# Kernel optimization log

Measured on AMD Instinct MI355X. Metric: run time of the kernel, lower is better.

The kernel has to match this reference:

```python
import jax, jax.numpy as jnp
import numpy as np

D = 1024   # feature_dim
K = 10     # num_anchors
B = 16384  # batch
H = 8      # num_heads


def setup_inputs() -> dict:
    key = jax.random.key(0)
    ks = jax.random.split(key, 12)
    f32 = jnp.float32

    def w(k, shape, scale=0.02):
        return (jax.random.normal(k, shape, f32) * scale)

    return {
        "features": jax.random.normal(ks[0], (B, D), f32),
        "anchors": w(ks[1], (K, D), 0.1),
        # anchor_refiner: Linear(D, D//2) -> ReLU -> Linear(D//2, D) -> Tanh
        "ar_w1": w(ks[2], (D, D // 2)), "ar_b1": jnp.zeros((D // 2,), f32),
        "ar_w2": w(ks[3], (D // 2, D)), "ar_b2": jnp.zeros((D,), f32),
        # attention projections
        "q_w": w(ks[4], (D, D)), "q_b": jnp.zeros((D,), f32),
        "k_w": w(ks[5], (D, D)), "k_b": jnp.zeros((D,), f32),
        "v_w": w(ks[6], (D, D)), "v_b": jnp.zeros((D,), f32),
        "o_w": w(ks[7], (D, D)), "o_b": jnp.zeros((D,), f32),
        # feature_enhancer: LayerNorm -> Linear(D,2D) -> GELU -> Linear(2D,D)
        "ln_g": jnp.ones((D,), f32), "ln_b": jnp.zeros((D,), f32),
        "ff_w1": w(ks[8], (D, 2 * D)), "ff_b1": jnp.zeros((2 * D,), f32),
        "ff_w2": w(ks[9], (2 * D, D)), "ff_b2": jnp.zeros((D,), f32),
        "div_w": jnp.asarray(0.001, f32),
        "cen_w": jnp.asarray(0.001, f32),
    }


def _l2norm(x, eps=1e-8):
    n = jnp.linalg.norm(x, axis=-1, keepdims=True)
    return x / jnp.maximum(n, eps)


def _layernorm(x, g, b, eps=1e-5):
    mu = jnp.mean(x, axis=-1, keepdims=True)
    var = jnp.mean(jnp.square(x - mu), axis=-1, keepdims=True)
    return (x - mu) * jax.lax.rsqrt(var + eps) * g + b


def reference(features, anchors, ar_w1, ar_b1, ar_w2, ar_b2,
              q_w, q_b, k_w, k_b, v_w, v_b, o_w, o_b,
              ln_g, ln_b, ff_w1, ff_b1, ff_w2, ff_b2, div_w, cen_w):
    b = features.shape[0]
    hd = D // H
    fn = _l2norm(features)                                 # [B, D]

    # anchor refinement
    refin = jnp.tanh(jax.nn.relu(anchors @ ar_w1 + ar_b1) @ ar_w2 + ar_b2)
    an = _l2norm(anchors + 0.1 * refin)                    # [K, D]

    # multi-head cross-attention to anchors
    q = (fn @ q_w + q_b).reshape(b, H, hd)                 # [B, H, hd]
    k = (an @ k_w + k_b).reshape(K, H, hd)                 # [K, H, hd]
    v = (an @ v_w + v_b).reshape(K, H, hd)
    scores = jnp.einsum('bhd,khd->bhk', q, k) / jnp.sqrt(jnp.asarray(hd, fn.dtype))
    aw = jax.nn.softmax(scores, axis=-1)                   # [B, H, K]
    att = jnp.einsum('bhk,khd->bhd', aw, v).reshape(b, D)
    att = att @ o_w + o_b

    # feature enhancer (dropout inactive: eval mode)
    enh = fn + 0.1 * att
    h = jax.nn.gelu(_layernorm(enh, ln_g, ln_b) @ ff_w1 + ff_b1, approximate=False)
    enh = h @ ff_w2 + ff_b2
    final = fn + 0.2 * enh                                 # [B, D]

    # diversity loss: pdist over K=10 anchors (45 pairs)
    diff = an[:, None, :] - an[None, :, :]                 # [K, K, D]
    dmat = jnp.sqrt(jnp.maximum(jnp.sum(diff * diff, -1), 1e-24))
    iu = np.triu_indices(K, 1)
    div_loss = jnp.exp(-jnp.maximum(dmat[iu].mean(), 1e-6))

    # center loss: attention-weighted feature-anchor distances
    avg_att = aw.mean(axis=1)                              # [B, K]
    sq = (jnp.sum(fn * fn, 1, keepdims=True) + jnp.sum(an * an, 1)
          - 2.0 * fn @ an.T)
    fa_dist = jnp.sqrt(jnp.maximum(sq, 1e-12))             # [B, K]
    center_loss = jnp.sum(avg_att * fa_dist, axis=1).mean()

    geo = jnp.abs(div_w) * div_loss + jnp.abs(cen_w) * center_loss
    geo = jnp.clip(geo, 0.0, 0.01)
    return final, geo
```

## Files before the change

### kernel.cpp

```cpp
#include <hip/hip_runtime.h>
#include <hip/hip_bf16.h>
#include <math.h>

typedef __hip_bfloat16 bf16;

#define D_  1024
#define K_  10
#define B_  16384
#define H_  8
#define HD_ 128

struct alignas(16) BF8 { bf16 v[8]; };
struct alignas(8)  BF4 { bf16 v[4]; };

typedef __bf16 bf8v __attribute__((ext_vector_type(8)));
typedef float  f4v  __attribute__((ext_vector_type(4)));

__device__ __forceinline__ float b2f(bf16 x){ return __bfloat162float(x); }
__device__ __forceinline__ bf16  f2b(float x){ return __float2bfloat16(x); }

#define GL2LDS16(g, l) __builtin_amdgcn_global_load_lds( \
    (__attribute__((address_space(1))) void*)(g), \
    (__attribute__((address_space(3))) void*)(l), 16, 0, 0)

__global__ __launch_bounds__(256) void l2norm_k(const float* __restrict__ x,
                                                bf16* __restrict__ fnb) {
  int b = blockIdx.x, t = threadIdx.x;
  float4 v = ((const float4*)(x + (size_t)b * D_))[t];
  float p = v.x*v.x + v.y*v.y + v.z*v.z + v.w*v.w;
  #pragma unroll
  for (int o = 32; o > 0; o >>= 1) p += __shfl_down(p, o);
  __shared__ float wsum[4];
  if ((t & 63) == 0) wsum[t >> 6] = p;
  __syncthreads();
  __shared__ float inv_s;
  if (t == 0) inv_s = 1.f / fmaxf(sqrtf(wsum[0]+wsum[1]+wsum[2]+wsum[3]), 1e-8f);
  __syncthreads();
  float iv = inv_s;
  BF4 o;
  o.v[0] = f2b(v.x*iv); o.v[1] = f2b(v.y*iv);
  o.v[2] = f2b(v.z*iv); o.v[3] = f2b(v.w*iv);
  ((BF4*)(fnb + (size_t)b * D_))[t] = o;
}

__global__ __launch_bounds__(256) void wt_k(const float* __restrict__ w,
                                            bf16* __restrict__ wt, int R, int C) {
  __shared__ float tle[32][33];
  int c0 = blockIdx.x * 32, r0 = blockIdx.y * 32;
  int tx = threadIdx.x & 31, ty = threadIdx.x >> 5;
  #pragma unroll
  for (int i = 0; i < 32; i += 8)
    tle[ty + i][tx] = w[(size_t)(r0 + ty + i) * C + c0 + tx];
  __syncthreads();
  #pragma unroll
  for (int i = 0; i < 32; i += 8)
    wt[(size_t)(c0 + ty + i) * R + r0 + tx] = f2b(tle[tx][ty + i]);
}

template<int COLS, int KD, int ACT>
__global__ __launch_bounds__(256) void panelmm_k(
    const float* __restrict__ A, const float* __restrict__ W,
    const float* __restrict__ bias, const float* __restrict__ aux,
    float* __restrict__ out,
    const float* __restrict__ W2, const float* __restrict__ bias2,
    float* __restrict__ out2, int N, int npanel) {
  constexpr int GROUPS = 256 / COLS;
  constexpr int DCH = KD / GROUPS;
  __shared__ float A_s[K_][KD];
  __shared__ float part[K_][COLS][GROUPS];
  const int t = threadIdx.x;
  int blk = blockIdx.x;
  const float* Wm = W; const float* bm = bias; float* om = out;
  if (blk >= npanel) { blk -= npanel; Wm = W2; bm = bias2; om = out2; }
  const int panel = blk;
  for (int i = t; i < K_*KD; i += 256) A_s[0][i] = A[i];
  __syncthreads();
  const int cg = t % COLS, g = t / COLS;
  const int col = panel*COLS + cg;
  float s[K_];
  #pragma unroll
  for (int r = 0; r < K_; ++r) s[r] = 0.f;
  const float* wp = Wm + (size_t)(g*DCH)*N + col;
  for (int d = g*DCH; d < (g+1)*DCH; ++d) {
    float wv = *wp; wp += N;
    #pragma unroll
    for (int r = 0; r < K_; ++r) s[r] = fmaf(A_s[r][d], wv, s[r]);
  }
  #pragma unroll
  for (int r = 0; r < K_; ++r) part[r][cg][g] = s[r];
  __syncthreads();
  for (int o = t; o < K_*COLS; o += 256) {
    int r = o / COLS, c = o % COLS;
    float v = 0.f;
    #pragma unroll
    for (int gg = 0; gg < GROUPS; ++gg) v += part[r][c][gg];
    v += bm[panel*COLS + c];
    if constexpr (ACT == 1) v = fmaxf(v, 0.f);
    if constexpr (ACT == 2) v = aux[(size_t)r*N + panel*COLS + c] + 0.1f*tanhf(v);
    om[(size_t)r*N + panel*COLS + c] = v;
  }
}

template<int TRANSOUT, typename TW>
__global__ __launch_bounds__(256) void smallmm_k(
    const float* __restrict__ A, const TW* __restrict__ W,
    bf16* __restrict__ outb, float scale) {
  constexpr int COLS = 64, GROUPS = 4, DCH = 32, NW = 1024;
  __shared__ float A_s[K_][128];
  __shared__ float part[K_][COLS][GROUPS];
  const int t = threadIdx.x;
  const int h = blockIdx.x & 7, panel = blockIdx.x >> 3;
  for (int i = t; i < K_*128; i += 256) {
    int r = i >> 7, j = i & 127;
    A_s[r][j] = A[r*1024 + h*128 + j];
  }
  __syncthreads();
  const int cg = t % COLS, g = t / COLS;
  const int col = panel*COLS + cg;
  float s[K_];
  #pragma unroll
  for (int r = 0; r < K_; ++r) s[r] = 0.f;
  const TW* wp = W + (size_t)(h*128 + g*DCH)*NW + col;
  for (int d = g*DCH; d < g*DCH + DCH; ++d) {
    float wv;
    if constexpr (sizeof(TW) == 2) wv = b2f(*wp); else wv = *wp;
    wp += NW;
    #pragma unroll
    for (int r = 0; r < K_; ++r) s[r] = fmaf(A_s[r][d], wv, s[r]);
  }
  #pragma unroll
  for (int r = 0; r < K_; ++r) part[r][cg][g] = s[r];
  __syncthreads();
  for (int o = t; o < 16*COLS; o += 256) {
    int r = o / COLS, c = o % COLS;
    float v = 0.f;
    if (r < K_) {
      #pragma unroll
      for (int gg = 0; gg < GROUPS; ++gg) v += part[r][c][gg];
      v *= scale;
    }
    if constexpr (TRANSOUT) outb[(size_t)(panel*COLS + c)*128 + h*16 + r] = f2b(v);
    else                    outb[(size_t)(h*16 + r)*NW + panel*COLS + c] = f2b(v);
  }
}

__global__ void sbias_k(const float* __restrict__ qb, const float* __restrict__ Km,
                        float* __restrict__ sb) {
  int c = threadIdx.x;
  int h = c >> 4, k = c & 15;
  float s = 0.f;
  if (k < K_) {
    for (int j = 0; j < HD_; ++j)
      s = fmaf(qb[h*HD_ + j], Km[(size_t)k*D_ + h*HD_ + j], s);
  }
  sb[c] = s * 0.08838834764831845f;
}

__global__ __launch_bounds__(256) void ar3_k(const float* __restrict__ an_un,
    float* __restrict__ an, float* __restrict__ na, float* __restrict__ divloss) {
  __shared__ float a_s[K_][D_];
  __shared__ float nrm[K_];
  __shared__ float dm[45];
  const int t = threadIdx.x;
  for (int i = t; i < K_*D_; i += 256) a_s[0][i] = an_un[i];
  __syncthreads();
  const int wid = t >> 6, lane = t & 63;
  for (int r = wid; r < K_; r += 4) {
    float p = 0.f;
    for (int j = lane; j < D_; j += 64) p += a_s[r][j]*a_s[r][j];
    #pragma unroll
    for (int o = 1; o < 64; o <<= 1) p += __shfl_xor(p, o);
    if (lane == 0) nrm[r] = p;
  }
  __syncthreads();
  for (int i = t; i < K_*D_; i += 256) {
    int r = i >> 10;
    float iv = 1.f / fmaxf(sqrtf(nrm[r]), 1e-8f);
    float v = a_s[0][i] * iv;
    a_s[0][i] = v;
    an[i] = v;
  }
  if (t < K_) {
    float iv = 1.f / fmaxf(sqrtf(nrm[t]), 1e-8f);
    na[t] = nrm[t] * iv * iv;
  }
  __syncthreads();
  const int pr = t >> 2, sub = t & 3;
  if (pr < 45) {
    int i = 0, j = 0, c = pr;
    for (i = 0; i < K_; ++i) { int cnt = K_-1-i; if (c < cnt) { j = i+1+c; break; } c -= cnt; }
    float s = 0.f;
    for (int d = sub*256; d < sub*256 + 256; ++d) {
      float df = a_s[i][d] - a_s[j][d]; s += df*df;
    }
    s += __shfl_xor(s, 1); s += __shfl_xor(s, 2);
    if (sub == 0) dm[pr] = sqrtf(fmaxf(s, 1e-24f));
  }
  __syncthreads();
  if (t == 0) {
    float m = 0.f;
    for (int p = 0; p < 45; ++p) m += dm[p];
    m *= (1.f/45.f);
    *divloss = expf(-fmaxf(m, 1e-6f));
  }
}

template<int EPI, typename TO>
__global__ __launch_bounds__(256) void mgemm_k(
    const bf16* __restrict__ A, const bf16* __restrict__ Bt,
    const float* __restrict__ bias, const bf16* __restrict__ aux,
    TO* __restrict__ out, int M, int N, int Kd, float scale) {
  constexpr int BM = 128, BN = 128, BK = 32;
  __shared__ bf16 As[BM][BK];
  __shared__ bf16 Bs[BN][BK];
  const int tid = threadIdx.x;
  const int nMB = M / BM;
  const int nwg = gridDim.x;
  int wg = blockIdx.x;
  wg = (wg & 7) * (nwg >> 3) + (wg >> 3);
  const int mb = wg % nMB, nb = wg / nMB;
  const int bm = mb * BM, bn = nb * BN;

  const int srow = tid >> 2;
  const int sk   = (tid & 3) * 8;
  const bf16* ga = A  + (size_t)(bm + srow) * Kd + sk;
  const bf16* gb = Bt + (size_t)(bn + srow) * Kd + sk;
  const size_t rstep = (size_t)64 * Kd;
  bf16* la = &As[0][0] + tid * 8;
  bf16* lb = &Bs[0][0] + tid * 8;

  const int w    = tid >> 6;
  const int lane = tid & 63;
  const int wr = (w >> 1) * 64, wc = (w & 1) * 64;
  const int fr = lane & 15, fg = lane >> 4;

  f4v acc[4][4];
  const f4v zz = {0.f, 0.f, 0.f, 0.f};
  #pragma unroll
  for (int m = 0; m < 4; ++m)
    #pragma unroll
    for (int n = 0; n < 4; ++n) acc[m][n] = zz;

  for (int k0 = 0; k0 < Kd; k0 += BK) {
    GL2LDS16(ga,         la);
    GL2LDS16(ga + rstep, la + 2048);
    GL2LDS16(gb,         lb);
    GL2LDS16(gb + rstep, lb + 2048);
    __syncthreads();
    bf8v af[4], bf_[4];
    #pragma unroll
    for (int m = 0; m < 4; ++m)
      af[m] = *(const bf8v*)&As[wr + m*16 + fr][fg*8];
    #pragma unroll
    for (int n = 0; n < 4; ++n)
      bf_[n] = *(const bf8v*)&Bs[wc + n*16 + fr][fg*8];
    #pragma unroll
    for (int m = 0; m < 4; ++m)
      #pragma unroll
      for (int n = 0; n < 4; ++n)
        acc[m][n] = __builtin_amdgcn_mfma_f32_16x16x32_bf16(af[m], bf_[n], acc[m][n], 0, 0, 0);
    __syncthreads();
    ga += BK; gb += BK;
  }

  float bv[4];
  #pragma unroll
  for (int n = 0; n < 4; ++n) bv[n] = bias[bn + wc + n*16 + fr];
  #pragma unroll
  for (int m = 0; m < 4; ++m) {
    #pragma unroll
    for (int r = 0; r < 4; ++r) {
      const int row = bm + wr + m*16 + fg*4 + r;
      #pragma unroll
      for (int n = 0; n < 4; ++n) {
        const int col = bn + wc + n*16 + fr;
        float x = acc[m][n][r] + bv[n];
        if constexpr (EPI == 1) x = b2f(aux[(size_t)row * N + col]) + scale * x;
        if constexpr (EPI == 2) x = 0.5f * x * (1.f + erff(x * 0.70710678118654752f));
        if constexpr (sizeof(TO) == 2) out[(size_t)row * N + col] = f2b(x);
        else                           out[(size_t)row * N + col] = x;
      }
    }
  }
}

__device__ __forceinline__ BF8 pack8(float4 a, float4 b){
  BF8 o;
  o.v[0]=f2b(a.x); o.v[1]=f2b(a.y); o.v[2]=f2b(a.z); o.v[3]=f2b(a.w);
  o.v[4]=f2b(b.x); o.v[5]=f2b(b.y); o.v[6]=f2b(b.z); o.v[7]=f2b(b.w);
  return o;
}

__global__ __launch_bounds__(256) void attn2_k(
    const float* __restrict__ S, const bf16* __restrict__ fn,
    const float* __restrict__ an, const float* __restrict__ na,
    bf16* __restrict__ awp, float* __restrict__ cen_acc) {
  __shared__ bf16 Ab[K_][D_];
  __shared__ float na_s[K_];
  __shared__ float cred[4];
  const int t = threadIdx.x;
  for (int i = t*8; i < K_*D_; i += 2048) {
    float4 a0 = *(const float4*)(an+i), a1 = *(const float4*)(an+i+4);
    *(BF8*)(&Ab[0][0]+i) = pack8(a0, a1);
  }
  if (t < K_) na_s[t] = na[t];
  __syncthreads();
  const int wid = t >> 6, lane = t & 63;
  const int d0 = lane * 16;
  const int sub = lane & 7, head = lane >> 3;
  const int k0 = sub*2, k1 = k0 + 1;
  float na0 = (k0 < K_) ? na_s[k0] : 0.f;
  float na1 = (k1 < K_) ? na_s[k1] : 0.f;
  float c_acc = 0.f;
  const int row0 = blockIdx.x * 32 + wid * 8;

  for (int i = 0; i < 8; ++i) {
    const int row = row0 + i;
    float2 sv = *(const float2*)(S + (size_t)row*128 + head*16 + k0);
    float v0 = (k0 < K_) ? sv.x : -1e30f;
    float v1 = (k1 < K_) ? sv.y : -1e30f;
    float m = fmaxf(v0, v1);
    m = fmaxf(m, __shfl_xor(m,1)); m = fmaxf(m, __shfl_xor(m,2)); m = fmaxf(m, __shfl_xor(m,4));
    float e0 = (k0 < K_) ? __expf(v0 - m) : 0.f;
    float e1 = (k1 < K_) ? __expf(v1 - m) : 0.f;
    float es = e0 + e1;
    es += __shfl_xor(es,1); es += __shfl_xor(es,2); es += __shfl_xor(es,4);
    float inv = 1.f / es;
    float a0 = e0 * inv, a1 = e1 * inv;
    bf16 b0 = f2b(a0), b1 = f2b(a1);
    unsigned int pk = (unsigned int)(*(unsigned short*)&b0)
                    | ((unsigned int)(*(unsigned short*)&b1) << 16);
    *(unsigned int*)(awp + (size_t)row*128 + head*16 + k0) = pk;
    float g0 = a0, g1 = a1;
    g0 += __shfl_xor(g0,8); g0 += __shfl_xor(g0,16); g0 += __shfl_xor(g0,32);
    g1 += __shfl_xor(g1,8); g1 += __shfl_xor(g1,16); g1 += __shfl_xor(g1,32);
    const BF8* fr = (const BF8*)(fn + (size_t)row*D_) + lane*2;
    BF8 f0 = fr[0], f1 = fr[1];
    float fv[16];
    #pragma unroll
    for (int j = 0; j < 8; ++j) { fv[j] = b2f(f0.v[j]); fv[8+j] = b2f(f1.v[j]); }
    float my0 = 0.f, my1 = 0.f;
    #pragma unroll
    for (int k = 0; k < K_; ++k) {
      BF8 aa = *(const BF8*)&Ab[k][d0];
      BF8 ab = *(const BF8*)&Ab[k][d0 + 8];
      float s = 0.f;
      #pragma unroll
      for (int j = 0; j < 8; ++j) {
        s = fmaf(fv[j],   b2f(aa.v[j]), s);
        s = fmaf(fv[8+j], b2f(ab.v[j]), s);
      }
      #pragma unroll
      for (int o = 1; o < 64; o <<= 1) s += __shfl_xor(s, o);
      my0 = (k == k0) ? s : my0;
      my1 = (k == k1) ? s : my1;
    }
    if (sub < 5) {
      float dist0 = sqrtf(fmaxf(1.f + na0 - 2.f*my0, 1e-12f));
      float dist1 = sqrtf(fmaxf(1.f + na1 - 2.f*my1, 1e-12f));
      c_acc = fmaf(g0, dist0, c_acc);
      c_acc = fmaf(g1, dist1, c_acc);
    }
  }
  #pragma unroll
  for (int o = 1; o < 64; o <<= 1) c_acc += __shfl_xor(c_acc, o);
  if (lane == 0) cred[wid] = c_acc;
  __syncthreads();
  if (t == 0) {
    float s = (cred[0]+cred[1]+cred[2]+cred[3]) * (1.f/64.f/(float)B_);
    atomicAdd(cen_acc, s);
  }
}

__global__ __launch_bounds__(256) void ln_k(const bf16* __restrict__ x,
    const float* __restrict__ g, const float* __restrict__ bta,
    bf16* __restrict__ out) {
  int b = blockIdx.x, t = threadIdx.x;
  BF4 ld = ((const BF4*)(x + (size_t)b * D_))[t];
  float v[4];
  #pragma unroll
  for (int j = 0; j < 4; ++j) v[j] = b2f(ld.v[j]);
  float s = v[0]+v[1]+v[2]+v[3];
  #pragma unroll
  for (int o = 32; o > 0; o >>= 1) s += __shfl_down(s, o);
  __shared__ float w1[4], w2[4];
  if ((t & 63) == 0) w1[t >> 6] = s;
  __syncthreads();
  __shared__ float mu_s, rs_s;
  if (t == 0) mu_s = (w1[0]+w1[1]+w1[2]+w1[3]) * (1.f/D_);
  __syncthreads();
  float mu = mu_s;
  float qv = 0.f;
  #pragma unroll
  for (int j = 0; j < 4; ++j) { float d = v[j]-mu; qv += d*d; }
  #pragma unroll
  for (int o = 32; o > 0; o >>= 1) qv += __shfl_down(qv, o);
  if ((t & 63) == 0) w2[t >> 6] = qv;
  __syncthreads();
  if (t == 0) rs_s = rsqrtf((w2[0]+w2[1]+w2[2]+w2[3]) * (1.f/D_) + 1e-5f);
  __syncthreads();
  float rs = rs_s;
  BF4 o;
  #pragma unroll
  for (int j = 0; j < 4; ++j) {
    int col = t*4 + j;
    o.v[j] = f2b((v[j]-mu)*rs*g[col] + bta[col]);
  }
  ((BF4*)(out + (size_t)b * D_))[t] = o;
}

__global__ void geo_k(const float* __restrict__ divl, const float* __restrict__ cen,
                      const float* __restrict__ div_w, const float* __restrict__ cen_w,
                      float* __restrict__ out) {
  float g = fabsf(*div_w) * (*divl) + fabsf(*cen_w) * (*cen);
  out[0] = fminf(fmaxf(g, 0.f), 0.01f);
}

extern "C" void kernel_launch(void* const* d_in, const int* in_sizes, int n_in,
                              void* d_out, int out_size, void* d_ws, size_t ws_size,
                              hipStream_t stream) {
  const float* features = (const float*)d_in[0];
  const float* anchors  = (const float*)d_in[1];
  const float* ar_w1 = (const float*)d_in[2];
  const float* ar_b1 = (const float*)d_in[3];
  const float* ar_w2 = (const float*)d_in[4];
  const float* ar_b2 = (const float*)d_in[5];
  const float* q_w = (const float*)d_in[6];
  const float* q_b = (const float*)d_in[7];
  const float* k_w = (const float*)d_in[8];
  const float* k_b = (const float*)d_in[9];
  const float* v_w = (const float*)d_in[10];
  const float* v_b = (const float*)d_in[11];
  const float* o_w = (const float*)d_in[12];
  const float* o_b = (const float*)d_in[13];
  const float* ln_g = (const float*)d_in[14];
  const float* ln_b = (const float*)d_in[15];
  const float* ff_w1 = (const float*)d_in[16];
  const float* ff_b1 = (const float*)d_in[17];
  const float* ff_w2 = (const float*)d_in[18];
  const float* ff_b2 = (const float*)d_in[19];
  const float* div_w = (const float*)d_in[20];
  const float* cen_w = (const float*)d_in[21];
  float* out = (float*)d_out;

  char* w = (char*)d_ws;
  bf16* ws_fnb = (bf16*)w;  w += (size_t)B_ * D_ * 2;
  bf16* ws_enh = (bf16*)w;  w += (size_t)B_ * D_ * 2;
  bf16* ws_ln  = (bf16*)w;  w += (size_t)B_ * D_ * 2;
  bf16* ws_h   = (bf16*)w;  w += (size_t)B_ * 2048 * 2;
  float* ws_S  = (float*)w; w += (size_t)B_ * 128 * 4;
  bf16* ws_awp = (bf16*)w;  w += (size_t)B_ * 128 * 2;
  bf16* ws_wq  = (bf16*)w;  w += (size_t)D_ * D_ * 2;
  bf16* ws_w1t = (bf16*)w;  w += (size_t)D_ * 2048 * 2;
  bf16* ws_w2t = (bf16*)w;  w += (size_t)2048 * D_ * 2;
  bf16* ws_wt  = (bf16*)w;  w += (size_t)128 * D_ * 2;
  bf16* ws_vt  = (bf16*)w;  w += (size_t)D_ * 128 * 2;
  float* ws_har = (float*)w;  w += (size_t)K_ * (D_/2) * 4;
  float* ws_anu = (float*)w;  w += (size_t)K_ * D_ * 4;
  float* ws_an  = (float*)w;  w += (size_t)K_ * D_ * 4;
  float* ws_k   = (float*)w;  w += (size_t)K_ * D_ * 4;
  float* ws_v   = (float*)w;  w += (size_t)K_ * D_ * 4;
  float* ws_na  = (float*)w;  w += 256;
  float* ws_div = (float*)w;  w += 256;
  float* ws_cen = (float*)w;  w += 256;
  float* ws_sb  = (float*)w;  w += 512;
  if ((size_t)(w - (char*)d_ws) > ws_size) return;

  hipMemsetAsync(ws_cen, 0, 4, stream);

  wt_k<<<dim3(D_/32,   D_/32),   256, 0, stream>>>(q_w,   ws_wq,  D_,   D_);
  wt_k<<<dim3(2048/32, D_/32),   256, 0, stream>>>(ff_w1, ws_w1t, D_,   2048);
  wt_k<<<dim3(D_/32,   2048/32), 256, 0, stream>>>(ff_w2, ws_w2t, 2048, D_);

  l2norm_k<<<B_, 256, 0, stream>>>(features, ws_fnb);

  panelmm_k<32, 1024, 1><<<16, 256, 0, stream>>>(
      anchors, ar_w1, ar_b1, nullptr, ws_har,
      nullptr, nullptr, nullptr, D_/2, 16);
  panelmm_k<64, 512, 2><<<16, 256, 0, stream>>>(
      ws_har, ar_w2, ar_b2, anchors, ws_anu,
      nullptr, nullptr, nullptr, D_, 16);
  ar3_k<<<1, 256, 0, stream>>>(ws_anu, ws_an, ws_na, ws_div);
  panelmm_k<64, 1024, 0><<<32, 256, 0, stream>>>(
      ws_an, k_w, k_b, nullptr, ws_k,
      v_w, v_b, ws_v, D_, 16);

  smallmm_k<0, bf16><<<128, 256, 0, stream>>>(ws_k, ws_wq, ws_wt, 0.08838834764831845f);
  sbias_k<<<1, 128, 0, stream>>>(q_b, ws_k, ws_sb);
  smallmm_k<1, float><<<128, 256, 0, stream>>>(ws_v, o_w, ws_vt, 1.f);

  mgemm_k<0, float><<<dim3((B_/128)*(128/128)), 256, 0, stream>>>(
      ws_fnb, ws_wt, ws_sb, nullptr, ws_S, B_, 128, D_, 0.f);

  attn2_k<<<B_/32, 256, 0, stream>>>(ws_S, ws_fnb, ws_an, ws_na, ws_awp, ws_cen);

  mgemm_k<1, bf16><<<dim3((B_/128)*(D_/128)), 256, 0, stream>>>(
      ws_awp, ws_vt, o_b, ws_fnb, ws_enh, B_, D_, 128, 0.1f);

  ln_k<<<B_, 256, 0, stream>>>(ws_enh, ln_g, ln_b, ws_ln);

  mgemm_k<2, bf16><<<dim3((B_/128)*(2048/128)), 256, 0, stream>>>(
      ws_ln, ws_w1t, ff_b1, nullptr, ws_h, B_, 2048, D_, 0.f);

  mgemm_k<1, float><<<dim3((B_/128)*(D_/128)), 256, 0, stream>>>(
      ws_h, ws_w2t, ff_b2, ws_fnb, out, B_, D_, 2048, 0.2f);

  geo_k<<<1, 1, 0, stream>>>(ws_div, ws_cen, div_w, cen_w, out + (size_t)B_ * D_);
}
```

Measured before the change: 476.0 us.

## Add 256x256-tile triple-buffered MFMA GEMM for output and FFN projections

Adds a new GEMM kernel using 256x256 output tiles with 512 threads, a 3-deep LDS ring buffer filled by direct global-to-LDS loads, explicit vmcnt waits, and s_setprio around the MFMA block. The o-projection and both feed-forward GEMMs now use it in place of the 128x128 kernel. The goal is more operand reuse per LDS tile and better overlap of memory loads with compute. In exchange it uses much more LDS and registers per workgroup, and launches fewer workgroups; the K=128 o-projection has only four k-steps, so there is little to pipeline there.

```diff
diff --git a/kernel.cpp b/kernel.cpp
--- a/kernel.cpp
+++ b/kernel.cpp
@@ -274,6 +274,108 @@
       #pragma unroll
       for (int n = 0; n < 4; ++n) {
         const int col = bn + wc + n*16 + fr;
+        float x = acc[m][n][r] + bv[n];
+        if constexpr (EPI == 1) x = b2f(aux[(size_t)row * N + col]) + scale * x;
+        if constexpr (EPI == 2) x = 0.5f * x * (1.f + erff(x * 0.70710678118654752f));
+        if constexpr (sizeof(TO) == 2) out[(size_t)row * N + col] = f2b(x);
+        else                           out[(size_t)row * N + col] = x;
+      }
+    }
+  }
+}
+
+template<int EPI, typename TO>
+__global__ __launch_bounds__(512, 2) void mgemm256_k(
+    const bf16* __restrict__ A, const bf16* __restrict__ Bt,
+    const float* __restrict__ bias, const bf16* __restrict__ aux,
+    TO* __restrict__ out, int M, int N, int Kd, float scale) {
+  constexpr int BM = 256, BN = 256, BK = 32, DEPTH = 3;
+  __shared__ bf16 As[DEPTH][BM*BK];
+  __shared__ bf16 Bs[DEPTH][BN*BK];
+  const int tid = threadIdx.x;
+  const int nMB = M / BM;
+  const int nwg = gridDim.x;
+  int wg = blockIdx.x;
+  wg = (wg & 7) * (nwg >> 3) + (wg >> 3);
+  const int bm = (wg % nMB) * BM, bn = (wg / nMB) * BN;
+
+  const int sr = tid >> 2, ss = tid & 3;
+  const int sx = ((ss ^ (sr & 3)) * 8);
+  const bf16* gA0 = A  + (size_t)(bm + sr)       * Kd + sx;
+  const bf16* gA1 = A  + (size_t)(bm + sr + 128) * Kd + sx;
+  const bf16* gB0 = Bt + (size_t)(bn + sr)       * Kd + sx;
+  const bf16* gB1 = Bt + (size_t)(bn + sr + 128) * Kd + sx;
+
+  const int wid = tid >> 6, lane = tid & 63;
+  const int wm = wid >> 2, wn = wid & 3;
+  const int fr = lane & 15, fg = lane >> 4;
+  const int slot = (fg ^ (fr & 3)) * 8;
+
+  f4v acc[8][4];
+  const f4v zz = {0.f, 0.f, 0.f, 0.f};
+  #pragma unroll
+  for (int m = 0; m < 8; ++m)
+    #pragma unroll
+    for (int n = 0; n < 4; ++n) acc[m][n] = zz;
+
+  const int nt = Kd / BK;
+  #pragma unroll
+  for (int p = 0; p < DEPTH; ++p) {
+    const int ko = p * BK;
+    GL2LDS16(gA0 + ko, &As[p][0] + tid*8);
+    GL2LDS16(gA1 + ko, &As[p][0] + tid*8 + 4096);
+    GL2LDS16(gB0 + ko, &Bs[p][0] + tid*8);
+    GL2LDS16(gB1 + ko, &Bs[p][0] + tid*8 + 4096);
+  }
+
+  int bufi = 0;
+  for (int t = 0; t < nt; ++t) {
+    const int rem = nt - 1 - t;
+    if (rem >= 2)      asm volatile("s_waitcnt vmcnt(8)" ::: "memory");
+    else if (rem == 1) asm volatile("s_waitcnt vmcnt(4)" ::: "memory");
+    else               asm volatile("s_waitcnt vmcnt(0)" ::: "memory");
+    __builtin_amdgcn_s_barrier();
+    asm volatile("" ::: "memory");
+    const bf16* la = &As[bufi][0];
+    const bf16* lb = &Bs[bufi][0];
+    bf8v af[8], bq[4];
+    #pragma unroll
+    for (int m = 0; m < 8; ++m)
+      af[m] = *(const bf8v*)(la + (wm*128 + m*16 + fr)*BK + slot);
+    #pragma unroll
+    for (int n = 0; n < 4; ++n)
+      bq[n] = *(const bf8v*)(lb + (wn*64 + n*16 + fr)*BK + slot);
+    asm volatile("s_waitcnt lgkmcnt(0)" ::: "memory");
+    __builtin_amdgcn_s_barrier();
+    asm volatile("" ::: "memory");
+    if (t + DEPTH < nt) {
+      const int ko = (t + DEPTH) * BK;
+      GL2LDS16(gA0 + ko, &As[bufi][0] + tid*8);
+      GL2LDS16(gA1 + ko, &As[bufi][0] + tid*8 + 4096);
+      GL2LDS16(gB0 + ko, &Bs[bufi][0] + tid*8);
+      GL2LDS16(gB1 + ko, &Bs[bufi][0] + tid*8 + 4096);
+    }
+    __builtin_amdgcn_s_setprio(1);
+    #pragma unroll
+    for (int m = 0; m < 8; ++m)
+      #pragma unroll
+      for (int n = 0; n < 4; ++n)
+        acc[m][n] = __builtin_amdgcn_mfma_f32_16x16x32_bf16(af[m], bq[n], acc[m][n], 0, 0, 0);
+    __builtin_amdgcn_s_setprio(0);
+    bufi = (bufi == DEPTH-1) ? 0 : bufi + 1;
+  }
+
+  float bv[4];
+  #pragma unroll
+  for (int n = 0; n < 4; ++n) bv[n] = bias[bn + wn*64 + n*16 + fr];
+  #pragma unroll
+  for (int m = 0; m < 8; ++m) {
+    #pragma unroll
+    for (int r = 0; r < 4; ++r) {
+      const int row = bm + wm*128 + m*16 + fg*4 + r;
+      #pragma unroll
+      for (int n = 0; n < 4; ++n) {
+        const int col = bn + wn*64 + n*16 + fr;
         float x = acc[m][n][r] + bv[n];
         if constexpr (EPI == 1) x = b2f(aux[(size_t)row * N + col]) + scale * x;
         if constexpr (EPI == 2) x = 0.5f * x * (1.f + erff(x * 0.70710678118654752f));
@@ -494,15 +596,15 @@
 
   attn2_k<<<B_/32, 256, 0, stream>>>(ws_S, ws_fnb, ws_an, ws_na, ws_awp, ws_cen);
 
-  mgemm_k<1, bf16><<<dim3((B_/128)*(D_/128)), 256, 0, stream>>>(
+  mgemm256_k<1, bf16><<<dim3((B_/256)*(D_/256)), 512, 0, stream>>>(
       ws_awp, ws_vt, o_b, ws_fnb, ws_enh, B_, D_, 128, 0.1f);
 
   ln_k<<<B_, 256, 0, stream>>>(ws_enh, ln_g, ln_b, ws_ln);
 
-  mgemm_k<2, bf16><<<dim3((B_/128)*(2048/128)), 256, 0, stream>>>(
+  mgemm256_k<2, bf16><<<dim3((B_/256)*(2048/256)), 512, 0, stream>>>(
       ws_ln, ws_w1t, ff_b1, nullptr, ws_h, B_, 2048, D_, 0.f);
 
-  mgemm_k<1, float><<<dim3((B_/128)*(D_/128)), 256, 0, stream>>>(
+  mgemm256_k<1, float><<<dim3((B_/256)*(D_/256)), 512, 0, stream>>>(
       ws_h, ws_w2t, ff_b2, ws_fnb, out, B_, D_, 2048, 0.2f);
 
   geo_k<<<1, 1, 0, stream>>>(ws_div, ws_cen, div_w, cen_w, out + (size_t)B_ * D_);
```

Result: faster. 446.1 us (-6.3%).
